# Optimization experiments

Measured on AMD Instinct MI355X. Metric: run time of the kernel, lower is better.

## Reference

```python
import jax, jax.numpy as jnp
import numpy as np

N = 100000
E = 1600000
HID = 128
EPS = 1e-8


def _linear_params(key, fan_in, fan_out, bias=True, gain=1.0):
    kw, kb = jax.random.split(key)
    bound = gain / np.sqrt(fan_in)
    W = jax.random.uniform(kw, (fan_in, fan_out), jnp.float32, -bound, bound)
    if bias:
        b = jax.random.uniform(kb, (fan_out,), jnp.float32, -bound, bound)
        return W, b
    return W


def setup_inputs() -> dict:
    key = jax.random.key(0)
    ks = jax.random.split(key, 12)
    h = jax.random.normal(ks[0], (N, HID), jnp.float32)
    coord = jax.random.normal(ks[1], (N, 3), jnp.float32)
    edge_index = jax.random.randint(ks[2], (2, E), 0, N, jnp.int64)
    # edge_mlp: Linear(2*HID+1 -> HID), SiLU, Linear(HID -> HID), SiLU
    We1, be1 = _linear_params(ks[3], 2 * HID + 1, HID)
    We2, be2 = _linear_params(ks[4], HID, HID)
    # node_mlp: Linear(2*HID -> HID), SiLU, Linear(HID -> HID)
    Wn1, bn1 = _linear_params(ks[5], 2 * HID, HID)
    Wn2, bn2 = _linear_params(ks[6], HID, HID)
    # coord_mlp: Linear(HID -> HID), SiLU, Linear(HID -> 1, no bias, xavier gain=0.001)
    Wc1, bc1 = _linear_params(ks[7], HID, HID)
    Wc2 = _linear_params(ks[8], HID, 1, bias=False, gain=0.001 * np.sqrt(6.0 * HID / (HID + 1)))
    return {
        "h": h, "edge_index": edge_index, "coord": coord,
        "We1": We1, "be1": be1, "We2": We2, "be2": be2,
        "Wn1": Wn1, "bn1": bn1, "Wn2": Wn2, "bn2": bn2,
        "Wc1": Wc1, "bc1": bc1, "Wc2": Wc2,
    }


def _egcl(h, edge_index, coord, We1, be1, We2, be2, Wn1, bn1, Wn2, bn2, Wc1, bc1, Wc2):
    row, col = edge_index[0], edge_index[1]
    n = h.shape[0]
    # coord2radial (normalize=True, detach on norm)
    coord_diff = coord[row] - coord[col]                       # [E,3]
    radial = jnp.sum(coord_diff ** 2, axis=1, keepdims=True)   # [E,1]
    norm = jax.lax.stop_gradient(jnp.sqrt(radial)) + EPS
    coord_diff = coord_diff / norm
    # edge_model (no edge_attr, no attention)
    edge_in = jnp.concatenate([h[row], h[col], radial], axis=1)  # [E, 2H+1]
    m = jax.nn.silu(edge_in @ We1 + be1)
    m = jax.nn.silu(m @ We2 + be2)                               # [E,H]
    # coord_model (coords_agg='mean', tanh=False)
    phi_x = jax.nn.silu(m @ Wc1 + bc1) @ Wc2                     # [E,1]
    trans = coord_diff * phi_x                                   # [E,3]
    agg_c = jax.ops.segment_sum(trans, row, num_segments=n)
    cnt = jax.ops.segment_sum(jnp.ones((trans.shape[0],), trans.dtype), row, num_segments=n)
    agg_c = agg_c / jnp.clip(cnt, 1.0, None)[:, None]
    coord_out = coord + agg_c
    # node_model (residual=True)
    agg_h = jax.ops.segment_sum(m, row, num_segments=n)          # [N,H]
    node_in = jnp.concatenate([h, agg_h], axis=1)
    out = jax.nn.silu(node_in @ Wn1 + bn1) @ Wn2 + bn2
    h_out = h + out
    return h_out, coord_out


def reference(h, edge_index, coord, We1, be1, We2, be2, Wn1, bn1, Wn2, bn2, Wc1, bc1, Wc2):
    return _egcl(h, edge_index, coord, We1, be1, We2, be2, Wn1, bn1, Wn2, bn2, Wc1, bc1, Wc2)
```

## Files before the change

### kernel.cpp

```cpp
#include <hip/hip_runtime.h>

#define NN 100000
#define NE 1600000
#define HD 128
#define EPSV 1e-8f
#define EB 128
#define LPAD 136
#define CPAD 264

typedef unsigned short ushort_t;
typedef __attribute__((ext_vector_type(8))) short bf16x8;
typedef __attribute__((ext_vector_type(4))) float f32x4;

__device__ __forceinline__ float silu_f(float x) {
    return x * __builtin_amdgcn_rcpf(1.0f + __expf(-x));
}
__device__ __forceinline__ float b2f(unsigned short u) {
    union { unsigned int i; float f; } v; v.i = ((unsigned int)u) << 16; return v.f;
}
__device__ __forceinline__ unsigned short f2b(float f) {
    union { float f; unsigned int i; } v; v.f = f;
    unsigned int r = v.i + 0x7fff + ((v.i >> 16) & 1);
    return (unsigned short)(r >> 16);
}
__device__ __forceinline__ unsigned int cvt_pk_bf16(float lo, float hi) {
    unsigned int r;
    asm("v_cvt_pk_bf16_f32 %0, %1, %2" : "=v"(r) : "v"(lo), "v"(hi));
    return r;
}

extern "C" __global__ __launch_bounds__(256)
void k_prep(const float* __restrict__ We2, const float* __restrict__ Wc1,
            const float* __restrict__ We1, const float* __restrict__ Wn1,
            const float* __restrict__ Wn2,
            ushort_t* __restrict__ We2T, ushort_t* __restrict__ Wc1T,
            ushort_t* __restrict__ WabT, ushort_t* __restrict__ Wn1T,
            ushort_t* __restrict__ Wn2T)
{
    int id = blockIdx.x * 256 + threadIdx.x;
    if (id < 16384) {
        int n = id >> 7, k = id & 127;
        We2T[id] = f2b(We2[k * HD + n]);
    } else if (id < 32768) {
        int r = id - 16384; int n = r >> 7, k = r & 127;
        Wc1T[r] = f2b(Wc1[k * HD + n]);
    } else if (id < 65536) {
        int r = id - 32768; int j = r >> 7, k = r & 127;
        float v = (j < 128) ? We1[k * HD + j] : We1[(size_t)(128 + k) * HD + (j - 128)];
        WabT[r] = f2b(v);
    } else if (id < 98304) {
        int r = id - 65536; int j = r >> 8, k = r & 255;
        Wn1T[r] = f2b(Wn1[(size_t)k * HD + j]);
    } else if (id < 114688) {
        int r = id - 98304; int j = r >> 7, k = r & 127;
        Wn2T[r] = f2b(Wn2[k * HD + j]);
    }
}

extern "C" __global__ __launch_bounds__(256)
void k_hist(const int* __restrict__ ei, int* __restrict__ deg)
{
    int e = blockIdx.x * 256 + threadIdx.x;
    atomicAdd(&deg[ei[e]], 1);
}

extern "C" __global__ __launch_bounds__(1024)
void k_scan(const int* __restrict__ deg, int* __restrict__ cursor)
{
    __shared__ int wsum[16];
    __shared__ int carry_s;
    const int tid = threadIdx.x;
    const int lane = tid & 63, w = tid >> 6;
    if (tid == 0) carry_s = 0;
    __syncthreads();
    for (int base = 0; base < NN; base += 1024) {
        int i = base + tid;
        int v = (i < NN) ? deg[i] : 0;
        int s = v;
#pragma unroll
        for (int off = 1; off < 64; off <<= 1) {
            int t = __shfl_up(s, off, 64);
            if (lane >= off) s += t;
        }
        if (lane == 63) wsum[w] = s;
        __syncthreads();
        int carry = carry_s;
        if (w == 0) {
            int ws = (lane < 16) ? wsum[lane] : 0;
#pragma unroll
            for (int off = 1; off < 16; off <<= 1) {
                int t = __shfl_up(ws, off, 64);
                if (lane >= off) ws += t;
            }
            if (lane < 16) wsum[lane] = ws;
        }
        __syncthreads();
        int woff = (w == 0) ? 0 : wsum[w - 1];
        if (i < NN) cursor[i] = carry + woff + s - v;
        __syncthreads();
        if (tid == 0) carry_s = carry + wsum[15];
        __syncthreads();
    }
}

extern "C" __global__ __launch_bounds__(256)
void k_sortids(const int* __restrict__ ei, int* __restrict__ cursor,
               int* __restrict__ perm)
{
    int e = blockIdx.x * 256 + threadIdx.x;
    int slot = atomicAdd(&cursor[ei[e]], 1);
    perm[slot] = e;
}

extern "C" __global__ __launch_bounds__(256)
void k_ab(const float* __restrict__ h, const ushort_t* __restrict__ WabT,
          const float* __restrict__ be1,
          ushort_t* __restrict__ A, ushort_t* __restrict__ B)
{
    __shared__ ushort_t hs[64][LPAD] __attribute__((aligned(16)));
    const int tid = threadIdx.x;
    const int n0 = blockIdx.x * 64;
    {
        int r = tid >> 2, seg = tid & 3;
        int n = n0 + r; if (n >= NN) n = n0;
        const float4* src = (const float4*)(h + (size_t)n * HD + seg * 32);
        uint2* dst = (uint2*)&hs[r][seg * 32];
#pragma unroll
        for (int i = 0; i < 8; i++) {
            float4 v = src[i];
            uint2 p; p.x = cvt_pk_bf16(v.x, v.y); p.y = cvt_pk_bf16(v.z, v.w);
            dst[i] = p;
        }
    }
    __syncthreads();
    const int wave = tid >> 6, lane = tid & 63;
    const int lr = lane & 15, lg = lane >> 4;
    f32x4 acc[16];
#pragma unroll
    for (int nt = 0; nt < 16; nt++) acc[nt] = (f32x4){0.f, 0.f, 0.f, 0.f};
#pragma unroll
    for (int ks = 0; ks < 4; ks++) {
        bf16x8 af = *(const bf16x8*)&hs[wave * 16 + lr][ks * 32 + lg * 8];
#pragma unroll
        for (int nt = 0; nt < 16; nt++) {
            bf16x8 bf = *(const bf16x8*)(WabT + (size_t)(nt * 16 + lr) * HD + ks * 32 + lg * 8);
            acc[nt] = __builtin_amdgcn_mfma_f32_16x16x32_bf16(af, bf, acc[nt], 0, 0, 0);
        }
    }
#pragma unroll
    for (int nt = 0; nt < 16; nt++) {
        float bias = (nt < 8) ? be1[nt * 16 + lr] : 0.f;
#pragma unroll
        for (int r = 0; r < 4; r++) {
            int n = n0 + wave * 16 + lg * 4 + r;
            if (n < NN) {
                ushort_t v = f2b(acc[nt][r] + bias);
                if (nt < 8) A[(size_t)n * HD + nt * 16 + lr] = v;
                else        B[(size_t)n * HD + (nt - 8) * 16 + lr] = v;
            }
        }
    }
}

extern "C" __global__ __launch_bounds__(256, 4)
void k_edge(const int* __restrict__ ei, const int* __restrict__ perm,
            const float* __restrict__ coord,
            const ushort_t* __restrict__ A, const ushort_t* __restrict__ B,
            const float* __restrict__ WeL, const float* __restrict__ be2,
            const ushort_t* __restrict__ We2T,
            const ushort_t* __restrict__ Wc1T,
            const float* __restrict__ bc1, const float* __restrict__ Wc2,
            float* __restrict__ agg_h, float* __restrict__ agg_c)
{
    __shared__ ushort_t m_lds[EB][LPAD] __attribute__((aligned(16)));
    __shared__ float cd_lds[EB][4];
    __shared__ int rows_s[EB];

    const int tid = threadIdx.x;
    const int e  = tid >> 1;
    const int hf = tid & 1;
    const int ge = perm[blockIdx.x * EB + e];
    const int row = ei[ge];
    const int col = ei[NE + ge];

    float c0 = coord[(size_t)row * 3 + 0] - coord[(size_t)col * 3 + 0];
    float c1 = coord[(size_t)row * 3 + 1] - coord[(size_t)col * 3 + 1];
    float c2 = coord[(size_t)row * 3 + 2] - coord[(size_t)col * 3 + 2];
    float radial = c0 * c0 + c1 * c1 + c2 * c2;
    if (hf == 0) {
        rows_s[e] = row;
        float inv = __builtin_amdgcn_rcpf(sqrtf(radial) + EPSV);
        cd_lds[e][0] = c0 * inv; cd_lds[e][1] = c1 * inv; cd_lds[e][2] = c2 * inv;
    }

    {
        const bf16x8* A8 = (const bf16x8*)(A + (size_t)row * HD + hf * 64);
        const bf16x8* B8 = (const bf16x8*)(B + (size_t)col * HD + hf * 64);
        const float4* WL4 = (const float4*)WeL + hf * 16;
#pragma unroll
        for (int i = 0; i < 8; i++) {
            bf16x8 av = A8[i], bv = B8[i];
            float4 w0 = WL4[2 * i], w1 = WL4[2 * i + 1];
            float v0 = silu_f(b2f((ushort_t)av[0]) + b2f((ushort_t)bv[0]) + radial * w0.x);
            float v1 = silu_f(b2f((ushort_t)av[1]) + b2f((ushort_t)bv[1]) + radial * w0.y);
            float v2 = silu_f(b2f((ushort_t)av[2]) + b2f((ushort_t)bv[2]) + radial * w0.z);
            float v3 = silu_f(b2f((ushort_t)av[3]) + b2f((ushort_t)bv[3]) + radial * w0.w);
            float v4 = silu_f(b2f((ushort_t)av[4]) + b2f((ushort_t)bv[4]) + radial * w1.x);
            float v5 = silu_f(b2f((ushort_t)av[5]) + b2f((ushort_t)bv[5]) + radial * w1.y);
            float v6 = silu_f(b2f((ushort_t)av[6]) + b2f((ushort_t)bv[6]) + radial * w1.z);
            float v7 = silu_f(b2f((ushort_t)av[7]) + b2f((ushort_t)bv[7]) + radial * w1.w);
            uint4 p;
            p.x = cvt_pk_bf16(v0, v1); p.y = cvt_pk_bf16(v2, v3);
            p.z = cvt_pk_bf16(v4, v5); p.w = cvt_pk_bf16(v6, v7);
            *(uint4*)&m_lds[e][hf * 64 + i * 8] = p;
        }
    }

    const int wave = tid >> 6, lane = tid & 63;
    const int lr = lane & 15, lg = lane >> 4;

    f32x4 acc[2][8];
#pragma unroll
    for (int mt = 0; mt < 2; mt++)
#pragma unroll
        for (int nt = 0; nt < 8; nt++) acc[mt][nt] = (f32x4){0.f, 0.f, 0.f, 0.f};

#pragma unroll
    for (int ks = 0; ks < 4; ks++) {
        bf16x8 af0 = *(const bf16x8*)&m_lds[wave * 32 + lr][ks * 32 + lg * 8];
        bf16x8 af1 = *(const bf16x8*)&m_lds[wave * 32 + 16 + lr][ks * 32 + lg * 8];
#pragma unroll
        for (int nt = 0; nt < 8; nt++) {
            bf16x8 bf = *(const bf16x8*)(We2T + (size_t)(nt * 16 + lr) * HD + ks * 32 + lg * 8);
            acc[0][nt] = __builtin_amdgcn_mfma_f32_16x16x32_bf16(af0, bf, acc[0][nt], 0, 0, 0);
            acc[1][nt] = __builtin_amdgcn_mfma_f32_16x16x32_bf16(af1, bf, acc[1][nt], 0, 0, 0);
        }
    }

#pragma unroll
    for (int nt = 0; nt < 8; nt++) {
        float be2v = be2[nt * 16 + lr];
#pragma unroll
        for (int mt = 0; mt < 2; mt++)
#pragma unroll
            for (int r = 0; r < 4; r++) {
                int rrow = wave * 32 + mt * 16 + lg * 4 + r;
                m_lds[rrow][nt * 16 + lr] = f2b(silu_f(acc[mt][nt][r] + be2v));
            }
    }

#pragma unroll
    for (int mt = 0; mt < 2; mt++)
#pragma unroll
        for (int nt = 0; nt < 8; nt++) acc[mt][nt] = (f32x4){0.f, 0.f, 0.f, 0.f};

#pragma unroll
    for (int ks = 0; ks < 4; ks++) {
        bf16x8 af0 = *(const bf16x8*)&m_lds[wave * 32 + lr][ks * 32 + lg * 8];
        bf16x8 af1 = *(const bf16x8*)&m_lds[wave * 32 + 16 + lr][ks * 32 + lg * 8];
#pragma unroll
        for (int nt = 0; nt < 8; nt++) {
            bf16x8 bf = *(const bf16x8*)(Wc1T + (size_t)(nt * 16 + lr) * HD + ks * 32 + lg * 8);
            acc[0][nt] = __builtin_amdgcn_mfma_f32_16x16x32_bf16(af0, bf, acc[0][nt], 0, 0, 0);
            acc[1][nt] = __builtin_amdgcn_mfma_f32_16x16x32_bf16(af1, bf, acc[1][nt], 0, 0, 0);
        }
    }

    float ph[2][4];
#pragma unroll
    for (int mt = 0; mt < 2; mt++)
#pragma unroll
        for (int r = 0; r < 4; r++) ph[mt][r] = 0.f;
#pragma unroll
    for (int nt = 0; nt < 8; nt++) {
        float bc1v = bc1[nt * 16 + lr];
        float wc2v = Wc2[nt * 16 + lr];
#pragma unroll
        for (int mt = 0; mt < 2; mt++)
#pragma unroll
            for (int r = 0; r < 4; r++)
                ph[mt][r] += silu_f(acc[mt][nt][r] + bc1v) * wc2v;
    }
#pragma unroll
    for (int msk = 1; msk < 16; msk <<= 1)
#pragma unroll
        for (int mt = 0; mt < 2; mt++)
#pragma unroll
            for (int r = 0; r < 4; r++)
                ph[mt][r] += __shfl_xor(ph[mt][r], msk, 64);

    if (lr == 0) {
#pragma unroll
        for (int mt = 0; mt < 2; mt++)
#pragma unroll
            for (int r = 0; r < 4; r++) {
                int er = wave * 32 + mt * 16 + lg * 4 + r;
                float p = ph[mt][r];
                cd_lds[er][0] *= p; cd_lds[er][1] *= p; cd_lds[er][2] *= p;
            }
    }

    __syncthreads();

    {
        const int j = tid & 127, g = tid >> 7;
        const int es0 = g * 64, es1 = es0 + 64;
        float acc_r = 0.f;
        int cur = rows_s[es0];
        for (int es = es0; es < es1; es++) {
            int r = rows_s[es];
            if (r != cur) {
                atomicAdd(&agg_h[(size_t)cur * HD + j], acc_r);
                acc_r = 0.f; cur = r;
            }
            acc_r += b2f(m_lds[es][j]);
        }
        atomicAdd(&agg_h[(size_t)cur * HD + j], acc_r);
    }

    if (wave == 0) {
        int c = lane >> 4;
        int sub = lane & 15;
        if (c < 3) {
            const int es0 = sub * 8, es1 = es0 + 8;
            float acc_r = 0.f;
            int cur = rows_s[es0];
            for (int es = es0; es < es1; es++) {
                int r = rows_s[es];
                if (r != cur) {
                    atomicAdd(&agg_c[(size_t)cur * 3 + c], acc_r);
                    acc_r = 0.f; cur = r;
                }
                acc_r += cd_lds[es][c];
            }
            atomicAdd(&agg_c[(size_t)cur * 3 + c], acc_r);
        }
    }
}

extern "C" __global__ __launch_bounds__(256)
void k_node(const float* __restrict__ h, const ushort_t* __restrict__ Wn1T,
            const float* __restrict__ bn1, const ushort_t* __restrict__ Wn2T,
            const float* __restrict__ bn2, const float* __restrict__ coord,
            const int* __restrict__ deg,
            float* __restrict__ hout ,
            float* __restrict__ cout )
{
    __shared__ ushort_t cs[64][CPAD] __attribute__((aligned(16)));
    __shared__ ushort_t us[64][LPAD] __attribute__((aligned(16)));
    const int tid = threadIdx.x;
    const int n0 = blockIdx.x * 64;
    {
        int r = tid >> 2, seg = tid & 3;
        int n = n0 + r; if (n >= NN) n = n0;
        const float4* s0 = (const float4*)(h + (size_t)n * HD + seg * 32);
        const float4* s1 = (const float4*)(hout + (size_t)n * HD + seg * 32);
        uint2* d0 = (uint2*)&cs[r][seg * 32];
        uint2* d1 = (uint2*)&cs[r][128 + seg * 32];
#pragma unroll
        for (int i = 0; i < 8; i++) {
            float4 v = s0[i];
            uint2 p; p.x = cvt_pk_bf16(v.x, v.y); p.y = cvt_pk_bf16(v.z, v.w);
            d0[i] = p;
            float4 w = s1[i];
            uint2 q; q.x = cvt_pk_bf16(w.x, w.y); q.y = cvt_pk_bf16(w.z, w.w);
            d1[i] = q;
        }
    }
    __syncthreads();
    const int wave = tid >> 6, lane = tid & 63;
    const int lr = lane & 15, lg = lane >> 4;

    f32x4 acc[8];
#pragma unroll
    for (int nt = 0; nt < 8; nt++) acc[nt] = (f32x4){0.f, 0.f, 0.f, 0.f};
#pragma unroll
    for (int ks = 0; ks < 8; ks++) {
        bf16x8 af = *(const bf16x8*)&cs[wave * 16 + lr][ks * 32 + lg * 8];
#pragma unroll
        for (int nt = 0; nt < 8; nt++) {
            bf16x8 bf = *(const bf16x8*)(Wn1T + (size_t)(nt * 16 + lr) * 256 + ks * 32 + lg * 8);
            acc[nt] = __builtin_amdgcn_mfma_f32_16x16x32_bf16(af, bf, acc[nt], 0, 0, 0);
        }
    }
#pragma unroll
    for (int nt = 0; nt < 8; nt++) {
        float bn1v = bn1[nt * 16 + lr];
#pragma unroll
        for (int r = 0; r < 4; r++)
            us[wave * 16 + lg * 4 + r][nt * 16 + lr] = f2b(silu_f(acc[nt][r] + bn1v));
    }

#pragma unroll
    for (int nt = 0; nt < 8; nt++) acc[nt] = (f32x4){0.f, 0.f, 0.f, 0.f};
#pragma unroll
    for (int ks = 0; ks < 4; ks++) {
        bf16x8 af = *(const bf16x8*)&us[wave * 16 + lr][ks * 32 + lg * 8];
#pragma unroll
        for (int nt = 0; nt < 8; nt++) {
            bf16x8 bf = *(const bf16x8*)(Wn2T + (size_t)(nt * 16 + lr) * HD + ks * 32 + lg * 8);
            acc[nt] = __builtin_amdgcn_mfma_f32_16x16x32_bf16(af, bf, acc[nt], 0, 0, 0);
        }
    }
#pragma unroll
    for (int nt = 0; nt < 8; nt++) {
        float bn2v = bn2[nt * 16 + lr];
#pragma unroll
        for (int r = 0; r < 4; r++) {
            int n = n0 + wave * 16 + lg * 4 + r;
            if (n < NN) {
                size_t idx = (size_t)n * HD + nt * 16 + lr;
                hout[idx] = h[idx] + acc[nt][r] + bn2v;
            }
        }
    }

    if (tid < 64) {
        int n = n0 + tid;
        if (n < NN) {
            float invc = __builtin_amdgcn_rcpf(fmaxf((float)deg[n], 1.0f));
#pragma unroll
            for (int i = 0; i < 3; i++) {
                size_t idx = (size_t)n * 3 + i;
                cout[idx] = coord[idx] + cout[idx] * invc;
            }
        }
    }
}

extern "C" void kernel_launch(void* const* d_in, const int* in_sizes, int n_in,
                              void* d_out, int out_size, void* d_ws, size_t ws_size,
                              hipStream_t stream)
{
    const float* h     = (const float*)d_in[0];
    const int*   ei    = (const int*)d_in[1];
    const float* coord = (const float*)d_in[2];
    const float* We1   = (const float*)d_in[3];
    const float* be1   = (const float*)d_in[4];
    const float* We2   = (const float*)d_in[5];
    const float* be2   = (const float*)d_in[6];
    const float* Wn1   = (const float*)d_in[7];
    const float* bn1   = (const float*)d_in[8];
    const float* Wn2   = (const float*)d_in[9];
    const float* bn2   = (const float*)d_in[10];
    const float* Wc1   = (const float*)d_in[11];
    const float* bc1   = (const float*)d_in[12];
    const float* Wc2   = (const float*)d_in[13];

    float* out   = (float*)d_out;
    float* agg_h = out;
    float* agg_c = out + (size_t)NN * HD;

    ushort_t* A    = (ushort_t*)d_ws;
    ushort_t* B    = A + (size_t)NN * HD;
    ushort_t* We2T = B + (size_t)NN * HD;
    ushort_t* Wc1T = We2T + 16384;
    ushort_t* WabT = Wc1T + 16384;
    ushort_t* Wn1T = WabT + 32768;
    ushort_t* Wn2T = Wn1T + 32768;
    int* deg    = (int*)(Wn2T + 16384);
    int* cursor = deg + NN;
    int* perm   = cursor + NN;
    const float* WeL = We1 + (size_t)2 * HD * HD;

    hipMemsetAsync(d_out, 0, (size_t)out_size * sizeof(float), stream);
    hipMemsetAsync(deg, 0, (size_t)NN * sizeof(int), stream);

    k_prep<<<448, 256, 0, stream>>>(We2, Wc1, We1, Wn1, Wn2,
                                    We2T, Wc1T, WabT, Wn1T, Wn2T);
    k_hist<<<NE / 256, 256, 0, stream>>>(ei, deg);
    k_ab<<<(NN + 63) / 64, 256, 0, stream>>>(h, WabT, be1, A, B);
    k_scan<<<1, 1024, 0, stream>>>(deg, cursor);
    k_sortids<<<NE / 256, 256, 0, stream>>>(ei, cursor, perm);
    k_edge<<<NE / EB, 256, 0, stream>>>(ei, perm, coord, A, B, WeL, be2,
                                        We2T, Wc1T, bc1, Wc2, agg_h, agg_c);
    k_node<<<(NN + 63) / 64, 256, 0, stream>>>(h, Wn1T, bn1, Wn2T, bn2, coord,
                                               deg, agg_h, agg_c);
}
```

Measured before the change: 1.056 ms.

## Persistent edge kernel with prefetch, parallel scan, packed row/col sort, transposed MFMA epilogues

The edge kernel becomes persistent: 750 blocks each loop over 16-17 tiles and prefetch the next tile's row/col, coordinates and B rows while the current tile computes. The sort now writes packed (row,col) pairs, so the edge kernel no longer does an extra indirection through a permutation array. The single-block serial scan is replaced by a three-kernel parallel scan. The MFMA operands are swapped so each lane owns four consecutive columns, which gives vectorized bias loads, packed bf16 stores and float4 output stores in k_ab, k_edge and k_node. Occupancy hint drops to 3 blocks per CU, and the larger register state risks lower latency hiding.

```diff
diff --git a/kernel.cpp b/kernel.cpp
--- a/kernel.cpp
+++ b/kernel.cpp
@@ -5,6 +5,8 @@
 #define HD 128
 #define EPSV 1e-8f
 #define EB 128
+#define NTILES (NE / EB)
+#define EGRID 750
 #define LPAD 136
 #define CPAD 264
 
@@ -65,51 +67,83 @@
 }
 
 extern "C" __global__ __launch_bounds__(1024)
-void k_scan(const int* __restrict__ deg, int* __restrict__ cursor)
+void k_scan1(const int* __restrict__ deg, int* __restrict__ bsum)
 {
     __shared__ int wsum[16];
-    __shared__ int carry_s;
     const int tid = threadIdx.x;
     const int lane = tid & 63, w = tid >> 6;
-    if (tid == 0) carry_s = 0;
+    int i = blockIdx.x * 1024 + tid;
+    int v = (i < NN) ? deg[i] : 0;
+#pragma unroll
+    for (int off = 32; off > 0; off >>= 1) v += __shfl_xor(v, off, 64);
+    if (lane == 0) wsum[w] = v;
     __syncthreads();
-    for (int base = 0; base < NN; base += 1024) {
-        int i = base + tid;
-        int v = (i < NN) ? deg[i] : 0;
-        int s = v;
-#pragma unroll
-        for (int off = 1; off < 64; off <<= 1) {
-            int t = __shfl_up(s, off, 64);
-            if (lane >= off) s += t;
-        }
-        if (lane == 63) wsum[w] = s;
-        __syncthreads();
-        int carry = carry_s;
-        if (w == 0) {
-            int ws = (lane < 16) ? wsum[lane] : 0;
-#pragma unroll
-            for (int off = 1; off < 16; off <<= 1) {
-                int t = __shfl_up(ws, off, 64);
-                if (lane >= off) ws += t;
-            }
-            if (lane < 16) wsum[lane] = ws;
-        }
-        __syncthreads();
-        int woff = (w == 0) ? 0 : wsum[w - 1];
-        if (i < NN) cursor[i] = carry + woff + s - v;
-        __syncthreads();
-        if (tid == 0) carry_s = carry + wsum[15];
-        __syncthreads();
-    }
+    if (tid == 0) {
+        int s = 0;
+#pragma unroll
+        for (int k = 0; k < 16; k++) s += wsum[k];
+        bsum[blockIdx.x] = s;
+    }
+}
+
+extern "C" __global__ __launch_bounds__(128)
+void k_scan2(const int* __restrict__ bsum, int* __restrict__ boff, int nb)
+{
+    __shared__ int wsum2[2];
+    const int tid = threadIdx.x;
+    const int lane = tid & 63, w = tid >> 6;
+    int v = (tid < nb) ? bsum[tid] : 0;
+    int s = v;
+#pragma unroll
+    for (int off = 1; off < 64; off <<= 1) {
+        int t = __shfl_up(s, off, 64);
+        if (lane >= off) s += t;
+    }
+    if (lane == 63) wsum2[w] = s;
+    __syncthreads();
+    int excl = ((w == 1) ? wsum2[0] : 0) + s - v;
+    if (tid < nb) boff[tid] = excl;
+}
+
+extern "C" __global__ __launch_bounds__(1024)
+void k_scan3(const int* __restrict__ deg, const int* __restrict__ boff,
+             int* __restrict__ cursor)
+{
+    __shared__ int wsum[16];
+    const int tid = threadIdx.x;
+    const int lane = tid & 63, w = tid >> 6;
+    int i = blockIdx.x * 1024 + tid;
+    int v = (i < NN) ? deg[i] : 0;
+    int s = v;
+#pragma unroll
+    for (int off = 1; off < 64; off <<= 1) {
+        int t = __shfl_up(s, off, 64);
+        if (lane >= off) s += t;
+    }
+    if (lane == 63) wsum[w] = s;
+    __syncthreads();
+    if (w == 0) {
+        int ws = (lane < 16) ? wsum[lane] : 0;
+#pragma unroll
+        for (int off = 1; off < 16; off <<= 1) {
+            int t = __shfl_up(ws, off, 64);
+            if (lane >= off) ws += t;
+        }
+        if (lane < 16) wsum[lane] = ws;
+    }
+    __syncthreads();
+    int excl = boff[blockIdx.x] + ((w > 0) ? wsum[w - 1] : 0) + s - v;
+    if (i < NN) cursor[i] = excl;
 }
 
 extern "C" __global__ __launch_bounds__(256)
 void k_sortids(const int* __restrict__ ei, int* __restrict__ cursor,
-               int* __restrict__ perm)
+               int2* __restrict__ rc)
 {
     int e = blockIdx.x * 256 + threadIdx.x;
-    int slot = atomicAdd(&cursor[ei[e]], 1);
-    perm[slot] = e;
+    int r = ei[e], c = ei[NE + e];
+    int slot = atomicAdd(&cursor[r], 1);
+    rc[slot] = make_int2(r, c);
 }
 
 extern "C" __global__ __launch_bounds__(256)
@@ -140,31 +174,32 @@
     for (int nt = 0; nt < 16; nt++) acc[nt] = (f32x4){0.f, 0.f, 0.f, 0.f};
 #pragma unroll
     for (int ks = 0; ks < 4; ks++) {
-        bf16x8 af = *(const bf16x8*)&hs[wave * 16 + lr][ks * 32 + lg * 8];
+        bf16x8 hf8 = *(const bf16x8*)&hs[wave * 16 + lr][ks * 32 + lg * 8];
 #pragma unroll
         for (int nt = 0; nt < 16; nt++) {
-            bf16x8 bf = *(const bf16x8*)(WabT + (size_t)(nt * 16 + lr) * HD + ks * 32 + lg * 8);
-            acc[nt] = __builtin_amdgcn_mfma_f32_16x16x32_bf16(af, bf, acc[nt], 0, 0, 0);
-        }
-    }
-#pragma unroll
-    for (int nt = 0; nt < 16; nt++) {
-        float bias = (nt < 8) ? be1[nt * 16 + lr] : 0.f;
-#pragma unroll
-        for (int r = 0; r < 4; r++) {
-            int n = n0 + wave * 16 + lg * 4 + r;
-            if (n < NN) {
-                ushort_t v = f2b(acc[nt][r] + bias);
-                if (nt < 8) A[(size_t)n * HD + nt * 16 + lr] = v;
-                else        B[(size_t)n * HD + (nt - 8) * 16 + lr] = v;
-            }
-        }
-    }
-}
-
-extern "C" __global__ __launch_bounds__(256, 4)
-void k_edge(const int* __restrict__ ei, const int* __restrict__ perm,
-            const float* __restrict__ coord,
+            bf16x8 wf = *(const bf16x8*)(WabT + (size_t)(nt * 16 + lr) * HD + ks * 32 + lg * 8);
+            acc[nt] = __builtin_amdgcn_mfma_f32_16x16x32_bf16(wf, hf8, acc[nt], 0, 0, 0);
+        }
+    }
+    const int node = n0 + wave * 16 + lr;
+    if (node < NN) {
+#pragma unroll
+        for (int nt = 0; nt < 16; nt++) {
+            float4 bias = (nt < 8) ? ((const float4*)be1)[nt * 4 + lg]
+                                   : (float4){0.f, 0.f, 0.f, 0.f};
+            uint2 pk;
+            pk.x = cvt_pk_bf16(acc[nt][0] + bias.x, acc[nt][1] + bias.y);
+            pk.y = cvt_pk_bf16(acc[nt][2] + bias.z, acc[nt][3] + bias.w);
+            if (nt < 8)
+                *(uint2*)(A + (size_t)node * HD + nt * 16 + lg * 4) = pk;
+            else
+                *(uint2*)(B + (size_t)node * HD + (nt - 8) * 16 + lg * 4) = pk;
+        }
+    }
+}
+
+extern "C" __global__ __launch_bounds__(256, 3)
+void k_edge(const int2* __restrict__ rc, const float* __restrict__ coord,
             const ushort_t* __restrict__ A, const ushort_t* __restrict__ B,
             const float* __restrict__ WeL, const float* __restrict__ be2,
             const ushort_t* __restrict__ We2T,
@@ -179,162 +214,170 @@
     const int tid = threadIdx.x;
     const int e  = tid >> 1;
     const int hf = tid & 1;
-    const int ge = perm[blockIdx.x * EB + e];
-    const int row = ei[ge];
-    const int col = ei[NE + ge];
-
-    float c0 = coord[(size_t)row * 3 + 0] - coord[(size_t)col * 3 + 0];
-    float c1 = coord[(size_t)row * 3 + 1] - coord[(size_t)col * 3 + 1];
-    float c2 = coord[(size_t)row * 3 + 2] - coord[(size_t)col * 3 + 2];
-    float radial = c0 * c0 + c1 * c1 + c2 * c2;
-    if (hf == 0) {
-        rows_s[e] = row;
-        float inv = __builtin_amdgcn_rcpf(sqrtf(radial) + EPSV);
-        cd_lds[e][0] = c0 * inv; cd_lds[e][1] = c1 * inv; cd_lds[e][2] = c2 * inv;
-    }
-
-    {
-        const bf16x8* A8 = (const bf16x8*)(A + (size_t)row * HD + hf * 64);
-        const bf16x8* B8 = (const bf16x8*)(B + (size_t)col * HD + hf * 64);
-        const float4* WL4 = (const float4*)WeL + hf * 16;
-#pragma unroll
-        for (int i = 0; i < 8; i++) {
-            bf16x8 av = A8[i], bv = B8[i];
-            float4 w0 = WL4[2 * i], w1 = WL4[2 * i + 1];
-            float v0 = silu_f(b2f((ushort_t)av[0]) + b2f((ushort_t)bv[0]) + radial * w0.x);
-            float v1 = silu_f(b2f((ushort_t)av[1]) + b2f((ushort_t)bv[1]) + radial * w0.y);
-            float v2 = silu_f(b2f((ushort_t)av[2]) + b2f((ushort_t)bv[2]) + radial * w0.z);
-            float v3 = silu_f(b2f((ushort_t)av[3]) + b2f((ushort_t)bv[3]) + radial * w0.w);
-            float v4 = silu_f(b2f((ushort_t)av[4]) + b2f((ushort_t)bv[4]) + radial * w1.x);
-            float v5 = silu_f(b2f((ushort_t)av[5]) + b2f((ushort_t)bv[5]) + radial * w1.y);
-            float v6 = silu_f(b2f((ushort_t)av[6]) + b2f((ushort_t)bv[6]) + radial * w1.z);
-            float v7 = silu_f(b2f((ushort_t)av[7]) + b2f((ushort_t)bv[7]) + radial * w1.w);
-            uint4 p;
-            p.x = cvt_pk_bf16(v0, v1); p.y = cvt_pk_bf16(v2, v3);
-            p.z = cvt_pk_bf16(v4, v5); p.w = cvt_pk_bf16(v6, v7);
-            *(uint4*)&m_lds[e][hf * 64 + i * 8] = p;
-        }
-    }
-
     const int wave = tid >> 6, lane = tid & 63;
     const int lr = lane & 15, lg = lane >> 4;
 
-    f32x4 acc[2][8];
-#pragma unroll
-    for (int mt = 0; mt < 2; mt++)
-#pragma unroll
-        for (int nt = 0; nt < 8; nt++) acc[mt][nt] = (f32x4){0.f, 0.f, 0.f, 0.f};
-
-#pragma unroll
-    for (int ks = 0; ks < 4; ks++) {
-        bf16x8 af0 = *(const bf16x8*)&m_lds[wave * 32 + lr][ks * 32 + lg * 8];
-        bf16x8 af1 = *(const bf16x8*)&m_lds[wave * 32 + 16 + lr][ks * 32 + lg * 8];
+    const int b = blockIdx.x;
+    const int t0  = b * 16 + ((b < 500) ? b : 500);
+    const int ntl = (b < 500) ? 17 : 16;
+
+    int2 rc0 = rc[t0 * EB + e];
+    int row = rc0.x, col = rc0.y;
+    float crx = coord[(size_t)row * 3 + 0], cry = coord[(size_t)row * 3 + 1],
+          crz = coord[(size_t)row * 3 + 2];
+    float ccx = coord[(size_t)col * 3 + 0], ccy = coord[(size_t)col * 3 + 1],
+          ccz = coord[(size_t)col * 3 + 2];
+    bf16x8 Bst[8];
+    {
+        const bf16x8* Bp = (const bf16x8*)(B + (size_t)col * HD + hf * 64);
+#pragma unroll
+        for (int i = 0; i < 8; i++) Bst[i] = Bp[i];
+    }
+
+    for (int t = 0; t < ntl; t++) {
+        float c0 = crx - ccx, c1 = cry - ccy, c2 = crz - ccz;
+        float radial = c0 * c0 + c1 * c1 + c2 * c2;
+        if (hf == 0) {
+            rows_s[e] = row;
+            float inv = __builtin_amdgcn_rcpf(sqrtf(radial) + EPSV);
+            cd_lds[e][0] = c0 * inv; cd_lds[e][1] = c1 * inv; cd_lds[e][2] = c2 * inv;
+        }
+        {
+            const bf16x8* A8 = (const bf16x8*)(A + (size_t)row * HD + hf * 64);
+            const float4* WL4 = (const float4*)WeL + hf * 16;
+#pragma unroll
+            for (int i = 0; i < 8; i++) {
+                bf16x8 av = A8[i], bv = Bst[i];
+                float4 w0 = WL4[2 * i], w1 = WL4[2 * i + 1];
+                float v0 = silu_f(b2f((ushort_t)av[0]) + b2f((ushort_t)bv[0]) + radial * w0.x);
+                float v1 = silu_f(b2f((ushort_t)av[1]) + b2f((ushort_t)bv[1]) + radial * w0.y);
+                float v2 = silu_f(b2f((ushort_t)av[2]) + b2f((ushort_t)bv[2]) + radial * w0.z);
+                float v3 = silu_f(b2f((ushort_t)av[3]) + b2f((ushort_t)bv[3]) + radial * w0.w);
+                float v4 = silu_f(b2f((ushort_t)av[4]) + b2f((ushort_t)bv[4]) + radial * w1.x);
+                float v5 = silu_f(b2f((ushort_t)av[5]) + b2f((ushort_t)bv[5]) + radial * w1.y);
+                float v6 = silu_f(b2f((ushort_t)av[6]) + b2f((ushort_t)bv[6]) + radial * w1.z);
+                float v7 = silu_f(b2f((ushort_t)av[7]) + b2f((ushort_t)bv[7]) + radial * w1.w);
+                uint4 p;
+                p.x = cvt_pk_bf16(v0, v1); p.y = cvt_pk_bf16(v2, v3);
+                p.z = cvt_pk_bf16(v4, v5); p.w = cvt_pk_bf16(v6, v7);
+                *(uint4*)&m_lds[e][hf * 64 + i * 8] = p;
+            }
+        }
+        if (t + 1 < ntl) {
+            int2 rcn = rc[(t0 + t + 1) * EB + e];
+            row = rcn.x; col = rcn.y;
+            crx = coord[(size_t)row * 3 + 0]; cry = coord[(size_t)row * 3 + 1];
+            crz = coord[(size_t)row * 3 + 2];
+            ccx = coord[(size_t)col * 3 + 0]; ccy = coord[(size_t)col * 3 + 1];
+            ccz = coord[(size_t)col * 3 + 2];
+            const bf16x8* Bp = (const bf16x8*)(B + (size_t)col * HD + hf * 64);
+#pragma unroll
+            for (int i = 0; i < 8; i++) Bst[i] = Bp[i];
+        }
+
+        f32x4 acc[2][8];
+#pragma unroll
+        for (int mt = 0; mt < 2; mt++)
+#pragma unroll
+            for (int nt = 0; nt < 8; nt++) acc[mt][nt] = (f32x4){0.f, 0.f, 0.f, 0.f};
+#pragma unroll
+        for (int ks = 0; ks < 4; ks++) {
+            bf16x8 mf0 = *(const bf16x8*)&m_lds[wave * 32 + lr][ks * 32 + lg * 8];
+            bf16x8 mf1 = *(const bf16x8*)&m_lds[wave * 32 + 16 + lr][ks * 32 + lg * 8];
+#pragma unroll
+            for (int nt = 0; nt < 8; nt++) {
+                bf16x8 wf = *(const bf16x8*)(We2T + (size_t)(nt * 16 + lr) * HD + ks * 32 + lg * 8);
+                acc[0][nt] = __builtin_amdgcn_mfma_f32_16x16x32_bf16(wf, mf0, acc[0][nt], 0, 0, 0);
+                acc[1][nt] = __builtin_amdgcn_mfma_f32_16x16x32_bf16(wf, mf1, acc[1][nt], 0, 0, 0);
+            }
+        }
 #pragma unroll
         for (int nt = 0; nt < 8; nt++) {
-            bf16x8 bf = *(const bf16x8*)(We2T + (size_t)(nt * 16 + lr) * HD + ks * 32 + lg * 8);
-            acc[0][nt] = __builtin_amdgcn_mfma_f32_16x16x32_bf16(af0, bf, acc[0][nt], 0, 0, 0);
-            acc[1][nt] = __builtin_amdgcn_mfma_f32_16x16x32_bf16(af1, bf, acc[1][nt], 0, 0, 0);
-        }
-    }
-
-#pragma unroll
-    for (int nt = 0; nt < 8; nt++) {
-        float be2v = be2[nt * 16 + lr];
+            float4 be2v = ((const float4*)be2)[nt * 4 + lg];
+#pragma unroll
+            for (int mt = 0; mt < 2; mt++) {
+                float v0 = silu_f(acc[mt][nt][0] + be2v.x);
+                float v1 = silu_f(acc[mt][nt][1] + be2v.y);
+                float v2 = silu_f(acc[mt][nt][2] + be2v.z);
+                float v3 = silu_f(acc[mt][nt][3] + be2v.w);
+                uint2 pk; pk.x = cvt_pk_bf16(v0, v1); pk.y = cvt_pk_bf16(v2, v3);
+                *(uint2*)&m_lds[wave * 32 + mt * 16 + lr][nt * 16 + lg * 4] = pk;
+            }
+        }
+
 #pragma unroll
         for (int mt = 0; mt < 2; mt++)
 #pragma unroll
-            for (int r = 0; r < 4; r++) {
-                int rrow = wave * 32 + mt * 16 + lg * 4 + r;
-                m_lds[rrow][nt * 16 + lr] = f2b(silu_f(acc[mt][nt][r] + be2v));
-            }
-    }
-
-#pragma unroll
-    for (int mt = 0; mt < 2; mt++)
-#pragma unroll
-        for (int nt = 0; nt < 8; nt++) acc[mt][nt] = (f32x4){0.f, 0.f, 0.f, 0.f};
-
-#pragma unroll
-    for (int ks = 0; ks < 4; ks++) {
-        bf16x8 af0 = *(const bf16x8*)&m_lds[wave * 32 + lr][ks * 32 + lg * 8];
-        bf16x8 af1 = *(const bf16x8*)&m_lds[wave * 32 + 16 + lr][ks * 32 + lg * 8];
+            for (int nt = 0; nt < 8; nt++) acc[mt][nt] = (f32x4){0.f, 0.f, 0.f, 0.f};
+#pragma unroll
+        for (int ks = 0; ks < 4; ks++) {
+            bf16x8 mf0 = *(const bf16x8*)&m_lds[wave * 32 + lr][ks * 32 + lg * 8];
+            bf16x8 mf1 = *(const bf16x8*)&m_lds[wave * 32 + 16 + lr][ks * 32 + lg * 8];
+#pragma unroll
+            for (int nt = 0; nt < 8; nt++) {
+                bf16x8 wf = *(const bf16x8*)(Wc1T + (size_t)(nt * 16 + lr) * HD + ks * 32 + lg * 8);
+                acc[0][nt] = __builtin_amdgcn_mfma_f32_16x16x32_bf16(wf, mf0, acc[0][nt], 0, 0, 0);
+                acc[1][nt] = __builtin_amdgcn_mfma_f32_16x16x32_bf16(wf, mf1, acc[1][nt], 0, 0, 0);
+            }
+        }
+
+        float ph0 = 0.f, ph1 = 0.f;
 #pragma unroll
         for (int nt = 0; nt < 8; nt++) {
-            bf16x8 bf = *(const bf16x8*)(Wc1T + (size_t)(nt * 16 + lr) * HD + ks * 32 + lg * 8);
-            acc[0][nt] = __builtin_amdgcn_mfma_f32_16x16x32_bf16(af0, bf, acc[0][nt], 0, 0, 0);
-            acc[1][nt] = __builtin_amdgcn_mfma_f32_16x16x32_bf16(af1, bf, acc[1][nt], 0, 0, 0);
-        }
-    }
-
-    float ph[2][4];
-#pragma unroll
-    for (int mt = 0; mt < 2; mt++)
-#pragma unroll
-        for (int r = 0; r < 4; r++) ph[mt][r] = 0.f;
-#pragma unroll
-    for (int nt = 0; nt < 8; nt++) {
-        float bc1v = bc1[nt * 16 + lr];
-        float wc2v = Wc2[nt * 16 + lr];
-#pragma unroll
-        for (int mt = 0; mt < 2; mt++)
-#pragma unroll
-            for (int r = 0; r < 4; r++)
-                ph[mt][r] += silu_f(acc[mt][nt][r] + bc1v) * wc2v;
-    }
-#pragma unroll
-    for (int msk = 1; msk < 16; msk <<= 1)
-#pragma unroll
-        for (int mt = 0; mt < 2; mt++)
-#pragma unroll
-            for (int r = 0; r < 4; r++)
-                ph[mt][r] += __shfl_xor(ph[mt][r], msk, 64);
-
-    if (lr == 0) {
-#pragma unroll
-        for (int mt = 0; mt < 2; mt++)
-#pragma unroll
-            for (int r = 0; r < 4; r++) {
-                int er = wave * 32 + mt * 16 + lg * 4 + r;
-                float p = ph[mt][r];
-                cd_lds[er][0] *= p; cd_lds[er][1] *= p; cd_lds[er][2] *= p;
-            }
-    }
-
-    __syncthreads();
-
-    {
-        const int j = tid & 127, g = tid >> 7;
-        const int es0 = g * 64, es1 = es0 + 64;
-        float acc_r = 0.f;
-        int cur = rows_s[es0];
-        for (int es = es0; es < es1; es++) {
-            int r = rows_s[es];
-            if (r != cur) {
-                atomicAdd(&agg_h[(size_t)cur * HD + j], acc_r);
-                acc_r = 0.f; cur = r;
-            }
-            acc_r += b2f(m_lds[es][j]);
-        }
-        atomicAdd(&agg_h[(size_t)cur * HD + j], acc_r);
-    }
-
-    if (wave == 0) {
-        int c = lane >> 4;
-        int sub = lane & 15;
-        if (c < 3) {
-            const int es0 = sub * 8, es1 = es0 + 8;
+            float4 bc1v = ((const float4*)bc1)[nt * 4 + lg];
+            float4 wc2v = ((const float4*)Wc2)[nt * 4 + lg];
+            ph0 += silu_f(acc[0][nt][0] + bc1v.x) * wc2v.x
+                 + silu_f(acc[0][nt][1] + bc1v.y) * wc2v.y
+                 + silu_f(acc[0][nt][2] + bc1v.z) * wc2v.z
+                 + silu_f(acc[0][nt][3] + bc1v.w) * wc2v.w;
+            ph1 += silu_f(acc[1][nt][0] + bc1v.x) * wc2v.x
+                 + silu_f(acc[1][nt][1] + bc1v.y) * wc2v.y
+                 + silu_f(acc[1][nt][2] + bc1v.z) * wc2v.z
+                 + silu_f(acc[1][nt][3] + bc1v.w) * wc2v.w;
+        }
+        ph0 += __shfl_xor(ph0, 16, 64); ph0 += __shfl_xor(ph0, 32, 64);
+        ph1 += __shfl_xor(ph1, 16, 64); ph1 += __shfl_xor(ph1, 32, 64);
+        if (lg == 0) {
+            int e0 = wave * 32 + lr, e1 = e0 + 16;
+            cd_lds[e0][0] *= ph0; cd_lds[e0][1] *= ph0; cd_lds[e0][2] *= ph0;
+            cd_lds[e1][0] *= ph1; cd_lds[e1][1] *= ph1; cd_lds[e1][2] *= ph1;
+        }
+
+        __syncthreads();
+
+        {
+            const int j = tid & 127, g = tid >> 7;
+            const int es0 = g * 64, es1 = es0 + 64;
             float acc_r = 0.f;
             int cur = rows_s[es0];
             for (int es = es0; es < es1; es++) {
                 int r = rows_s[es];
                 if (r != cur) {
-                    atomicAdd(&agg_c[(size_t)cur * 3 + c], acc_r);
+                    atomicAdd(&agg_h[(size_t)cur * HD + j], acc_r);
                     acc_r = 0.f; cur = r;
                 }
-                acc_r += cd_lds[es][c];
-            }
-            atomicAdd(&agg_c[(size_t)cur * 3 + c], acc_r);
-        }
+                acc_r += b2f(m_lds[es][j]);
+            }
+            atomicAdd(&agg_h[(size_t)cur * HD + j], acc_r);
+        }
+        if (wave == 0) {
+            int c = lane >> 4, sub = lane & 15;
+            if (c < 3) {
+                const int es0 = sub * 8, es1 = es0 + 8;
+                float acc_r = 0.f;
+                int cur = rows_s[es0];
+                for (int es = es0; es < es1; es++) {
+                    int r = rows_s[es];
+                    if (r != cur) {
+                        atomicAdd(&agg_c[(size_t)cur * 3 + c], acc_r);
+                        acc_r = 0.f; cur = r;
+                    }
+                    acc_r += cd_lds[es][c];
+                }
+                atomicAdd(&agg_c[(size_t)cur * 3 + c], acc_r);
+            }
+        }
+        __syncthreads();
     }
 }
 
@@ -376,52 +419,55 @@
     for (int nt = 0; nt < 8; nt++) acc[nt] = (f32x4){0.f, 0.f, 0.f, 0.f};
 #pragma unroll
     for (int ks = 0; ks < 8; ks++) {
-        bf16x8 af = *(const bf16x8*)&cs[wave * 16 + lr][ks * 32 + lg * 8];
+        bf16x8 cf = *(const bf16x8*)&cs[wave * 16 + lr][ks * 32 + lg * 8];
 #pragma unroll
         for (int nt = 0; nt < 8; nt++) {
-            bf16x8 bf = *(const bf16x8*)(Wn1T + (size_t)(nt * 16 + lr) * 256 + ks * 32 + lg * 8);
-            acc[nt] = __builtin_amdgcn_mfma_f32_16x16x32_bf16(af, bf, acc[nt], 0, 0, 0);
+            bf16x8 wf = *(const bf16x8*)(Wn1T + (size_t)(nt * 16 + lr) * 256 + ks * 32 + lg * 8);
+            acc[nt] = __builtin_amdgcn_mfma_f32_16x16x32_bf16(wf, cf, acc[nt], 0, 0, 0);
         }
     }
 #pragma unroll
     for (int nt = 0; nt < 8; nt++) {
-        float bn1v = bn1[nt * 16 + lr];
-#pragma unroll
-        for (int r = 0; r < 4; r++)
-            us[wave * 16 + lg * 4 + r][nt * 16 + lr] = f2b(silu_f(acc[nt][r] + bn1v));
-    }
-
-#pragma unroll
-    for (int nt = 0; nt < 8; nt++) acc[nt] = (f32x4){0.f, 0.f, 0.f, 0.f};
+        float4 b1 = ((const float4*)bn1)[nt * 4 + lg];
+        float v0 = silu_f(acc[nt][0] + b1.x);
+        float v1 = silu_f(acc[nt][1] + b1.y);
+        float v2 = silu_f(acc[nt][2] + b1.z);
+        float v3 = silu_f(acc[nt][3] + b1.w);
+        uint2 pk; pk.x = cvt_pk_bf16(v0, v1); pk.y = cvt_pk_bf16(v2, v3);
+        *(uint2*)&us[wave * 16 + lr][nt * 16 + lg * 4] = pk;
+    }
+
+    f32x4 acc2[8];
+#pragma unroll
+    for (int nt = 0; nt < 8; nt++) acc2[nt] = (f32x4){0.f, 0.f, 0.f, 0.f};
 #pragma unroll
     for (int ks = 0; ks < 4; ks++) {
-        bf16x8 af = *(const bf16x8*)&us[wave * 16 + lr][ks * 32 + lg * 8];
+        bf16x8 uf = *(const bf16x8*)&us[wave * 16 + lr][ks * 32 + lg * 8];
 #pragma unroll
         for (int nt = 0; nt < 8; nt++) {
-            bf16x8 bf = *(const bf16x8*)(Wn2T + (size_t)(nt * 16 + lr) * HD + ks * 32 + lg * 8);
-            acc[nt] = __builtin_amdgcn_mfma_f32_16x16x32_bf16(af, bf, acc[nt], 0, 0, 0);
-        }
-    }
-#pragma unroll
-    for (int nt = 0; nt < 8; nt++) {
-        float bn2v = bn2[nt * 16 + lr];
-#pragma unroll
-        for (int r = 0; r < 4; r++) {
-            int n = n0 + wave * 16 + lg * 4 + r;
-            if (n < NN) {
-                size_t idx = (size_t)n * HD + nt * 16 + lr;
-                hout[idx] = h[idx] + acc[nt][r] + bn2v;
-            }
-        }
-    }
-
-    if (tid < 64) {
-        int n = n0 + tid;
-        if (n < NN) {
-            float invc = __builtin_amdgcn_rcpf(fmaxf((float)deg[n], 1.0f));
+            bf16x8 wf = *(const bf16x8*)(Wn2T + (size_t)(nt * 16 + lr) * HD + ks * 32 + lg * 8);
+            acc2[nt] = __builtin_amdgcn_mfma_f32_16x16x32_bf16(wf, uf, acc2[nt], 0, 0, 0);
+        }
+    }
+    const int node = n0 + wave * 16 + lr;
+    if (node < NN) {
+#pragma unroll
+        for (int nt = 0; nt < 8; nt++) {
+            float4 b2 = ((const float4*)bn2)[nt * 4 + lg];
+            size_t idx = (size_t)node * HD + nt * 16 + lg * 4;
+            float4 hv = *(const float4*)(h + idx);
+            float4 o;
+            o.x = hv.x + acc2[nt][0] + b2.x;
+            o.y = hv.y + acc2[nt][1] + b2.y;
+            o.z = hv.z + acc2[nt][2] + b2.z;
+            o.w = hv.w + acc2[nt][3] + b2.w;
+            *(float4*)(hout + idx) = o;
+        }
+        if (lg == 0) {
+            float invc = __builtin_amdgcn_rcpf(fmaxf((float)deg[node], 1.0f));
 #pragma unroll
             for (int i = 0; i < 3; i++) {
-                size_t idx = (size_t)n * 3 + i;
+                size_t idx = (size_t)node * 3 + i;
                 cout[idx] = coord[idx] + cout[idx] * invc;
             }
         }
@@ -460,8 +506,12 @@
     ushort_t* Wn2T = Wn1T + 32768;
     int* deg    = (int*)(Wn2T + 16384);
     int* cursor = deg + NN;
-    int* perm   = cursor + NN;
+    int* bsum   = cursor + NN;
+    int* boff   = bsum + 128;
+    int2* rc    = (int2*)(boff + 128);
     const float* WeL = We1 + (size_t)2 * HD * HD;
+
+    const int scan_nb = (NN + 1023) / 1024;
 
     hipMemsetAsync(d_out, 0, (size_t)out_size * sizeof(float), stream);
     hipMemsetAsync(deg, 0, (size_t)NN * sizeof(int), stream);
@@ -470,10 +520,12 @@
                                     We2T, Wc1T, WabT, Wn1T, Wn2T);
     k_hist<<<NE / 256, 256, 0, stream>>>(ei, deg);
     k_ab<<<(NN + 63) / 64, 256, 0, stream>>>(h, WabT, be1, A, B);
-    k_scan<<<1, 1024, 0, stream>>>(deg, cursor);
-    k_sortids<<<NE / 256, 256, 0, stream>>>(ei, cursor, perm);
-    k_edge<<<NE / EB, 256, 0, stream>>>(ei, perm, coord, A, B, WeL, be2,
-                                        We2T, Wc1T, bc1, Wc2, agg_h, agg_c);
+    k_scan1<<<scan_nb, 1024, 0, stream>>>(deg, bsum);
+    k_scan2<<<1, 128, 0, stream>>>(bsum, boff, scan_nb);
+    k_scan3<<<scan_nb, 1024, 0, stream>>>(deg, boff, cursor);
+    k_sortids<<<NE / 256, 256, 0, stream>>>(ei, cursor, rc);
+    k_edge<<<EGRID, 256, 0, stream>>>(rc, coord, A, B, WeL, be2,
+                                      We2T, Wc1T, bc1, Wc2, agg_h, agg_c);
     k_node<<<(NN + 63) / 64, 256, 0, stream>>>(h, Wn1T, bn1, Wn2T, bn2, coord,
                                                deg, agg_h, agg_c);
 }
```

Result: slower. 1.425 ms (+35.0%).
